# Performance work log

Measured on AMD Instinct MI355X. Metric: run time of the kernel, lower is better.

Reference implementation:

```python
import jax, jax.numpy as jnp
import numpy as np

N = 100000   # num_nodes
E = 300000   # num_edges
R = 200      # num_rels
B = 32       # num_bases (bdd blocks)
H = 128      # h_dim
SI = H // B  # submat_in = 4


def setup_inputs() -> dict:
    key = jax.random.key(0)
    ks = jax.random.split(key, 10)
    return {
        "node_ids": jnp.arange(N, dtype=jnp.int32),
        "src": jax.random.randint(ks[0], (E,), 0, N, dtype=jnp.int32),
        "dst": jax.random.randint(ks[1], (E,), 0, N, dtype=jnp.int32),
        "etypes": jax.random.randint(ks[2], (E,), 0, R, dtype=jnp.int32),
        "norm": jax.random.uniform(ks[3], (E, 1), dtype=jnp.float32),
        "emb": jax.random.normal(ks[4], (N, H), dtype=jnp.float32) * 0.02,
        "W1": jax.random.normal(ks[5], (R, B, SI, SI), dtype=jnp.float32) / np.float32(np.sqrt(SI)),
        "loop_w1": jax.random.normal(ks[6], (H, H), dtype=jnp.float32) / np.float32(np.sqrt(H)),
        "bias1": jnp.zeros((H,), dtype=jnp.float32),
        "W2": jax.random.normal(ks[7], (R, B, SI, 2 * SI), dtype=jnp.float32) / np.float32(np.sqrt(SI)),
        "loop_w2": jax.random.normal(ks[8], (H, 2 * H), dtype=jnp.float32) / np.float32(np.sqrt(H)),
        "bias2": jnp.zeros((2 * H,), dtype=jnp.float32),
        "eps": jax.random.normal(ks[9], (N, H), dtype=jnp.float32),
    }


def rel_graph_conv_bdd(h, src, dst, etypes, norm, W, loop_w, bias):
    """DGL RelGraphConv with regularizer='bdd', self_loop=True, bias=True."""
    _, Bb, si, so = W.shape
    h_src = h[src].reshape(-1, Bb, si)                  # (E, B, si)
    We = W[etypes]                                      # (E, B, si, so) gathered block weights
    msg = jnp.einsum('ebi,ebio->ebo', h_src, We).reshape(-1, Bb * so)  # (E, out)
    msg = msg * norm                                    # edge norm
    agg = jax.ops.segment_sum(msg, dst, num_segments=N)  # scatter-add to dst
    return agg + bias + h @ loop_w


def reference(node_ids, src, dst, etypes, norm, emb, W1, loop_w1, bias1, W2, loop_w2, bias2, eps):
    h = emb[node_ids]                                   # embedding lookup (N, H)
    h = jax.nn.relu(rel_graph_conv_bdd(h, src, dst, etypes, norm, W1, loop_w1, bias1))
    h = rel_graph_conv_bdd(h, src, dst, etypes, norm, W2, loop_w2, bias2)  # (N, 2H)
    # utils.gaussian_parameters: split last dim, v = softplus + 1e-8
    m, h_pre = jnp.split(h, 2, axis=-1)
    v = jax.nn.softplus(h_pre) + 1e-8
    # utils.sample_gaussian: reparameterized sample
    z = m + jnp.sqrt(v) * eps
    return z
```

## Files before the change

### kernel.cpp

```cpp
#include <hip/hip_runtime.h>
#include <math.h>

#define HD 128

union F4 { float4 v; float f[4]; };

typedef __attribute__((ext_vector_type(8))) short bf8_t;
typedef __attribute__((ext_vector_type(4))) float f4_t;

__device__ __forceinline__ unsigned short f2bf(float f){
  unsigned int u = __float_as_uint(f);
  return (unsigned short)((u + 0x7fffu + ((u>>16)&1u)) >> 16);
}

__device__ __forceinline__ float dotbf(const F4& h, unsigned int ua, unsigned int ub){
  float w0 = __uint_as_float(ua << 16);
  float w1 = __uint_as_float(ua & 0xffff0000u);
  float w2 = __uint_as_float(ub << 16);
  float w3 = __uint_as_float(ub & 0xffff0000u);
  return fmaf(h.f[0], w0, fmaf(h.f[1], w1, fmaf(h.f[2], w2, h.f[3]*w3)));
}

__device__ __forceinline__ void wpack_one(const float* __restrict__ W,
                                          unsigned short* __restrict__ Wp, int t, int NO){
  int lane = t & 63, ks = (t>>6) & 3, ct = t >> 8;
  int k0 = ks*32 + (lane>>4)*8, col = ct*16 + (lane&15);
  unsigned short v[8];
  #pragma unroll
  for (int j=0;j<8;++j) v[j] = f2bf(W[(k0+j)*NO + col]);
  ushort4* dst = (ushort4*)&Wp[(size_t)t*8];
  dst[0] = make_ushort4(v[0],v[1],v[2],v[3]);
  dst[1] = make_ushort4(v[4],v[5],v[6],v[7]);
}

__global__ void k_prep(const int* __restrict__ ids, const float4* __restrict__ emb4,
                       float4* __restrict__ h0, unsigned short* __restrict__ h0b,
                       const int* __restrict__ dst, int* __restrict__ counts,
                       const float* __restrict__ W1, unsigned short* __restrict__ W1Tb,
                       const float* __restrict__ W2, unsigned short* __restrict__ W2Tb,
                       const float* __restrict__ lw1, unsigned short* __restrict__ W1p,
                       const float* __restrict__ lw2, unsigned short* __restrict__ W2p,
                       int NG, int E, int n1, int n2){
  int i = blockIdx.x*256 + threadIdx.x;
  if (i < NG){
    int row = i>>5, c = i&31;
    float4 v = emb4[ids[row]*32 + c];
    h0[i] = v;
    *(ushort4*)&h0b[(size_t)i*4] = make_ushort4(f2bf(v.x),f2bf(v.y),f2bf(v.z),f2bf(v.w));
    return;
  }
  i -= NG;
  if (i < E){ atomicAdd(&counts[dst[i]], 1); return; }
  i -= E;
  if (i < n1){
    int ii = i & 3, o = (i>>2) & 3, rb = i>>4;
    W1Tb[i] = f2bf(W1[rb*16 + ii*4 + o]);
    return;
  }
  i -= n1;
  if (i < n2){
    int ii = i & 3, o = (i>>2) & 7, rb = i>>5;
    W2Tb[i] = f2bf(W2[rb*32 + ii*8 + o]);
    return;
  }
  i -= n2;
  if (i < 2048){ wpack_one(lw1, W1p, i, 128); return; }
  i -= 2048;
  if (i < 4096){ wpack_one(lw2, W2p, i, 256); }
}

__global__ void k_scan_block(const int* __restrict__ counts, int* __restrict__ scanTmp,
                             int* __restrict__ blockSums, int n){
  __shared__ int sm[256];
  int i = blockIdx.x*256 + threadIdx.x;
  int v = (i<n)?counts[i]:0;
  sm[threadIdx.x]=v; __syncthreads();
  for (int ofs=1; ofs<256; ofs<<=1){
    int t = (threadIdx.x>=ofs)?sm[threadIdx.x-ofs]:0;
    __syncthreads();
    sm[threadIdx.x]+=t;
    __syncthreads();
  }
  if (i<n) scanTmp[i]=sm[threadIdx.x];
  if (threadIdx.x==255) blockSums[blockIdx.x]=sm[255];
}

__global__ void k_scan_top(int* __restrict__ blockSums, int nb){
  __shared__ int sm[1024];
  int v = ((int)threadIdx.x<nb)?blockSums[threadIdx.x]:0;
  sm[threadIdx.x]=v; __syncthreads();
  for (int ofs=1; ofs<1024; ofs<<=1){
    int t = ((int)threadIdx.x>=ofs)?sm[threadIdx.x-ofs]:0;
    __syncthreads();
    sm[threadIdx.x]+=t;
    __syncthreads();
  }
  if ((int)threadIdx.x<nb) blockSums[threadIdx.x] = sm[threadIdx.x]-v;
}

__global__ void k_scan_fin(const int* __restrict__ scanTmp, const int* __restrict__ blockSums,
                           const int* __restrict__ counts,
                           int* __restrict__ row_ptr, int* __restrict__ cursors, int n){
  int i = blockIdx.x*256 + threadIdx.x;
  if (i<n){
    int incl = scanTmp[i] + blockSums[blockIdx.x];
    row_ptr[i+1] = incl;
    cursors[i] = incl - counts[i];
  }
  if (i==0) row_ptr[0]=0;
}

__global__ void k_scatter(const int* __restrict__ dst, const int* __restrict__ src,
                          const int* __restrict__ et, const float* __restrict__ norm,
                          int* __restrict__ cursors, int4* __restrict__ pay, int E){
  int e = blockIdx.x*256 + threadIdx.x;
  if (e<E){
    int p = atomicAdd(&cursors[dst[e]],1);
    pay[p] = make_int4(src[e], et[e], __float_as_int(norm[e]), 0);
  }
}

__global__ __launch_bounds__(256)
void k_edge1(const int* __restrict__ row_ptr, const int4* __restrict__ pay,
             const float* __restrict__ h, const unsigned short* __restrict__ WTb,
             float* __restrict__ agg, int Nn){
  int wid = __builtin_amdgcn_readfirstlane((blockIdx.x*256 + threadIdx.x)>>6);
  if (wid >= Nn) return;
  const int lane = threadIdx.x & 63;
  const int half = lane >> 5, b = lane & 31;
  const int e0 = row_ptr[wid], e1 = row_ptr[wid+1];
  float a0=0.f, a1=0.f, a2=0.f, a3=0.f;
  int e = e0 + half;
  int4 p;
  if (e < e1) p = pay[e];
  for (; e < e1; e += 2){
    int4 pn = (e+2 < e1) ? pay[e+2] : p;
    float nm = __int_as_float(p.z);
    F4 hv; hv.v = *(const float4*)&h[(size_t)p.x*HD + b*4];
    const uint4* wq = (const uint4*)&WTb[(size_t)p.y*512 + b*16];
    uint4 q0 = wq[0], q1 = wq[1];
    a0 = fmaf(nm, dotbf(hv, q0.x, q0.y), a0);
    a1 = fmaf(nm, dotbf(hv, q0.z, q0.w), a1);
    a2 = fmaf(nm, dotbf(hv, q1.x, q1.y), a2);
    a3 = fmaf(nm, dotbf(hv, q1.z, q1.w), a3);
    p = pn;
  }
  a0 += __shfl_xor(a0, 32); a1 += __shfl_xor(a1, 32);
  a2 += __shfl_xor(a2, 32); a3 += __shfl_xor(a3, 32);
  if (half == 0){
    F4 o; o.f[0]=a0; o.f[1]=a1; o.f[2]=a2; o.f[3]=a3;
    *(float4*)&agg[(size_t)wid*128 + b*4] = o.v;
  }
}

__global__ __launch_bounds__(256)
void k_edge2(const int* __restrict__ row_ptr, const int4* __restrict__ pay,
             const float* __restrict__ h, const unsigned short* __restrict__ WTb,
             float* __restrict__ agg, int Nn){
  int wid = __builtin_amdgcn_readfirstlane((blockIdx.x*256 + threadIdx.x)>>6);
  if (wid >= Nn) return;
  const int lane = threadIdx.x & 63;
  const int half = lane >> 5, b = lane & 31;
  const int e0 = row_ptr[wid], e1 = row_ptr[wid+1];
  float acc[8];
  #pragma unroll
  for (int o=0;o<8;++o) acc[o]=0.f;
  int e = e0 + half;
  int4 p;
  if (e < e1) p = pay[e];
  for (; e < e1; e += 2){
    int4 pn = (e+2 < e1) ? pay[e+2] : p;
    float nm = __int_as_float(p.z);
    F4 hv; hv.v = *(const float4*)&h[(size_t)p.x*HD + b*4];
    const uint4* wq = (const uint4*)&WTb[(size_t)p.y*1024 + b*32];
    uint4 q0 = wq[0], q1 = wq[1], q2 = wq[2], q3 = wq[3];
    acc[0] = fmaf(nm, dotbf(hv, q0.x, q0.y), acc[0]);
    acc[1] = fmaf(nm, dotbf(hv, q0.z, q0.w), acc[1]);
    acc[2] = fmaf(nm, dotbf(hv, q1.x, q1.y), acc[2]);
    acc[3] = fmaf(nm, dotbf(hv, q1.z, q1.w), acc[3]);
    acc[4] = fmaf(nm, dotbf(hv, q2.x, q2.y), acc[4]);
    acc[5] = fmaf(nm, dotbf(hv, q2.z, q2.w), acc[5]);
    acc[6] = fmaf(nm, dotbf(hv, q3.x, q3.y), acc[6]);
    acc[7] = fmaf(nm, dotbf(hv, q3.z, q3.w), acc[7]);
    p = pn;
  }
  #pragma unroll
  for (int o=0;o<8;++o) acc[o] += __shfl_xor(acc[o], 32);
  if (half == 0){
    F4 o0, o1;
    #pragma unroll
    for (int j=0;j<4;++j){ o0.f[j]=acc[j]; o1.f[j]=acc[4+j]; }
    *(float4*)&agg[(size_t)wid*256 + b*8]     = o0.v;
    *(float4*)&agg[(size_t)wid*256 + b*8 + 4] = o1.v;
  }
}

__global__ __launch_bounds__(256)
void k_mfma_relu(const unsigned short* __restrict__ Ab, const unsigned short* __restrict__ Wp,
                 const float* __restrict__ agg, const float* __restrict__ bias,
                 float* __restrict__ out, unsigned short* __restrict__ outb, int M){
  const int lane = threadIdx.x & 63;
  const int rowBase = blockIdx.x*64 + (threadIdx.x>>6)*16;
  const int ar = lane & 15, kg = lane >> 4;
  const int aclamp = min(rowBase + ar, M-1);
  f4_t acc[8];
  #pragma unroll
  for (int ct=0; ct<8; ++ct) acc[ct] = (f4_t)0.f;
  #pragma unroll
  for (int ks=0; ks<4; ++ks){
    bf8_t a = *(const bf8_t*)&Ab[(size_t)aclamp*HD + ks*32 + kg*8];
    #pragma unroll
    for (int ct=0; ct<8; ++ct){
      bf8_t b = *(const bf8_t*)&Wp[(size_t)((ct*4 + ks)*64 + lane)*8];
      acc[ct] = __builtin_amdgcn_mfma_f32_16x16x32_bf16(a, b, acc[ct], 0,0,0);
    }
  }
  const int crow = rowBase + kg*4;
  #pragma unroll
  for (int r=0; r<4; ++r){
    int gr = crow + r;
    if (gr >= M) continue;
    #pragma unroll
    for (int ct=0; ct<8; ++ct){
      int col = ct*16 + ar;
      float v = fmaxf(acc[ct][r] + agg[(size_t)gr*128 + col] + bias[col], 0.f);
      out[(size_t)gr*128 + col] = v;
      outb[(size_t)gr*128 + col] = f2bf(v);
    }
  }
}

__global__ __launch_bounds__(256)
void k_mfma_gauss(const unsigned short* __restrict__ Ab, const unsigned short* __restrict__ Wp,
                  const float* __restrict__ agg, const float* __restrict__ bias,
                  const float* __restrict__ eps, float* __restrict__ out, int M){
  const int lane = threadIdx.x & 63;
  const int bx = blockIdx.x & 1;
  const int rowBase = (blockIdx.x>>1)*64 + (threadIdx.x>>6)*16;
  const int ar = lane & 15, kg = lane >> 4;
  const int aclamp = min(rowBase + ar, M-1);
  f4_t accm[4], acch[4];
  #pragma unroll
  for (int ct=0; ct<4; ++ct){ accm[ct] = (f4_t)0.f; acch[ct] = (f4_t)0.f; }
  #pragma unroll
  for (int ks=0; ks<4; ++ks){
    bf8_t a = *(const bf8_t*)&Ab[(size_t)aclamp*HD + ks*32 + kg*8];
    #pragma unroll
    for (int ct=0; ct<4; ++ct){
      int ctm = bx*4 + ct, cth = 8 + bx*4 + ct;
      bf8_t bm = *(const bf8_t*)&Wp[(size_t)((ctm*4 + ks)*64 + lane)*8];
      bf8_t bh = *(const bf8_t*)&Wp[(size_t)((cth*4 + ks)*64 + lane)*8];
      accm[ct] = __builtin_amdgcn_mfma_f32_16x16x32_bf16(a, bm, accm[ct], 0,0,0);
      acch[ct] = __builtin_amdgcn_mfma_f32_16x16x32_bf16(a, bh, acch[ct], 0,0,0);
    }
  }
  const int crow = rowBase + kg*4;
  #pragma unroll
  for (int r=0; r<4; ++r){
    int gr = crow + r;
    if (gr >= M) continue;
    #pragma unroll
    for (int ct=0; ct<4; ++ct){
      int colm = bx*64 + ct*16 + ar;
      float m  = accm[ct][r] + agg[(size_t)gr*256 + colm]       + bias[colm];
      float hp = acch[ct][r] + agg[(size_t)gr*256 + colm + 128] + bias[colm+128];
      float sp = fmaxf(hp, 0.f) + log1pf(expf(-fabsf(hp)));
      out[(size_t)gr*128 + colm] = fmaf(sqrtf(sp + 1e-8f), eps[(size_t)gr*128 + colm], m);
    }
  }
}

extern "C" void kernel_launch(void* const* d_in, const int* in_sizes, int n_in,
                              void* d_out, int out_size, void* d_ws, size_t ws_size,
                              hipStream_t stream){
  (void)n_in; (void)out_size; (void)ws_size;
  const int*   node_ids = (const int*)d_in[0];
  const int*   src  = (const int*)d_in[1];
  const int*   dst  = (const int*)d_in[2];
  const int*   et   = (const int*)d_in[3];
  const float* norm = (const float*)d_in[4];
  const float* emb  = (const float*)d_in[5];
  const float* W1   = (const float*)d_in[6];
  const float* lw1  = (const float*)d_in[7];
  const float* b1   = (const float*)d_in[8];
  const float* W2   = (const float*)d_in[9];
  const float* lw2  = (const float*)d_in[10];
  const float* b2   = (const float*)d_in[11];
  const float* eps  = (const float*)d_in[12];
  float* out = (float*)d_out;

  const int N  = in_sizes[0];
  const int E  = in_sizes[1];
  const int n1 = in_sizes[6];
  const int n2 = in_sizes[9];

  char* w = (char*)d_ws;
  size_t szNH = (size_t)N*HD*sizeof(float);
  float* h0   = (float*)(w);
  float* agg2 = (float*)(w);
  float* h1   = (float*)(w + 2*szNH);
  float* agg1 = (float*)(w + 3*szNH);
  char*  ip   = w + 4*szNH;
  int4*  pay       = (int4*)ip;
  int*   counts    = (int*)(pay + E);
  int*   scanTmp   = counts + N;
  int*   row_ptr   = scanTmp + N;
  int*   cursors   = row_ptr + (N+1);
  int*   blockSums = cursors + N;
  size_t tail      = ((size_t)((char*)(blockSums + 1024) - w) + 63) & ~(size_t)63;
  unsigned short* W1Tb = (unsigned short*)(w + tail);
  unsigned short* W2Tb = W1Tb + n1;
  unsigned short* W1p  = W2Tb + n2;
  unsigned short* W2p  = W1p + 8*256*8;
  unsigned short* h0b  = W2p + 16*256*8;
  unsigned short* h1b  = h0b + (size_t)N*HD;

  hipMemsetAsync(counts, 0, (size_t)N*sizeof(int), stream);

  const int NG = N*32;
  const int Tprep = NG + E + n1 + n2 + 2048 + 4096;
  int nb_e    = (E+255)/256;
  int nb_scan = (N+255)/256;

  k_prep<<<(Tprep+255)/256, 256, 0, stream>>>(node_ids, (const float4*)emb, (float4*)h0, h0b,
                                              dst, counts, W1, W1Tb, W2, W2Tb,
                                              lw1, W1p, lw2, W2p, NG, E, n1, n2);
  k_scan_block<<<nb_scan, 256, 0, stream>>>(counts, scanTmp, blockSums, N);
  k_scan_top<<<1, 1024, 0, stream>>>(blockSums, nb_scan);
  k_scan_fin<<<nb_scan, 256, 0, stream>>>(scanTmp, blockSums, counts, row_ptr, cursors, N);
  k_scatter<<<nb_e, 256, 0, stream>>>(dst, src, et, norm, cursors, pay, E);

  int nb_rows = (N+3)/4;
  int nb_m    = (N+63)/64;

  k_edge1<<<nb_rows, 256, 0, stream>>>(row_ptr, pay, h0, W1Tb, agg1, N);
  k_mfma_relu<<<nb_m, 256, 0, stream>>>(h0b, W1p, agg1, b1, h1, h1b, N);
  k_edge2<<<nb_rows, 256, 0, stream>>>(row_ptr, pay, h1, W2Tb, agg2, N);
  k_mfma_gauss<<<nb_m*2, 256, 0, stream>>>(h1b, W2p, agg2, b2, eps, out, N);
}
```

Baseline: 435.4 us.

## Gather bf16 node features in edge kernels and process four edges per wave

The edge kernels now gather the bf16 copy of the node features instead of the fp32 copy. The fp32 h0/h1 buffers are no longer written, which removes a full fp32 write per layer and halves the bytes read per gathered row. The per-wave mapping changes from 2 edges × 32 lanes (4 channels each) to 4 edges × 16 lanes (8 channels each), with a two-step shuffle reduction. This trades some feature precision (bf16 instead of fp32 input to the messages) and adds more registers and weight loads per lane.

New measurement: 434.4 us. Within noise of the previous version (-0.2%).

```diff
diff --git a/kernel.cpp b/kernel.cpp
--- a/kernel.cpp
+++ b/kernel.cpp
@@ -12,13 +12,11 @@
   unsigned int u = __float_as_uint(f);
   return (unsigned short)((u + 0x7fffu + ((u>>16)&1u)) >> 16);
 }
+__device__ __forceinline__ float bflo(unsigned int u){ return __uint_as_float(u << 16); }
+__device__ __forceinline__ float bfhi(unsigned int u){ return __uint_as_float(u & 0xffff0000u); }
 
 __device__ __forceinline__ float dotbf(const F4& h, unsigned int ua, unsigned int ub){
-  float w0 = __uint_as_float(ua << 16);
-  float w1 = __uint_as_float(ua & 0xffff0000u);
-  float w2 = __uint_as_float(ub << 16);
-  float w3 = __uint_as_float(ub & 0xffff0000u);
-  return fmaf(h.f[0], w0, fmaf(h.f[1], w1, fmaf(h.f[2], w2, h.f[3]*w3)));
+  return fmaf(h.f[0], bflo(ua), fmaf(h.f[1], bfhi(ua), fmaf(h.f[2], bflo(ub), h.f[3]*bfhi(ub))));
 }
 
 __device__ __forceinline__ void wpack_one(const float* __restrict__ W,
@@ -34,7 +32,7 @@
 }
 
 __global__ void k_prep(const int* __restrict__ ids, const float4* __restrict__ emb4,
-                       float4* __restrict__ h0, unsigned short* __restrict__ h0b,
+                       unsigned short* __restrict__ h0b,
                        const int* __restrict__ dst, int* __restrict__ counts,
                        const float* __restrict__ W1, unsigned short* __restrict__ W1Tb,
                        const float* __restrict__ W2, unsigned short* __restrict__ W2Tb,
@@ -45,7 +43,6 @@
   if (i < NG){
     int row = i>>5, c = i&31;
     float4 v = emb4[ids[row]*32 + c];
-    h0[i] = v;
     *(ushort4*)&h0b[(size_t)i*4] = make_ushort4(f2bf(v.x),f2bf(v.y),f2bf(v.z),f2bf(v.w));
     return;
   }
@@ -122,83 +119,115 @@
 
 __global__ __launch_bounds__(256)
 void k_edge1(const int* __restrict__ row_ptr, const int4* __restrict__ pay,
-             const float* __restrict__ h, const unsigned short* __restrict__ WTb,
+             const unsigned short* __restrict__ h, const unsigned short* __restrict__ WTb,
              float* __restrict__ agg, int Nn){
   int wid = __builtin_amdgcn_readfirstlane((blockIdx.x*256 + threadIdx.x)>>6);
   if (wid >= Nn) return;
   const int lane = threadIdx.x & 63;
-  const int half = lane >> 5, b = lane & 31;
+  const int g = lane >> 4, l = lane & 15;
   const int e0 = row_ptr[wid], e1 = row_ptr[wid+1];
-  float a0=0.f, a1=0.f, a2=0.f, a3=0.f;
-  int e = e0 + half;
+  const int cnt = e1 - e0;
+  float acc[8];
+  #pragma unroll
+  for (int o=0;o<8;++o) acc[o]=0.f;
+  const int T = (cnt + 3) >> 2;
   int4 p;
-  if (e < e1) p = pay[e];
-  for (; e < e1; e += 2){
-    int4 pn = (e+2 < e1) ? pay[e+2] : p;
-    float nm = __int_as_float(p.z);
-    F4 hv; hv.v = *(const float4*)&h[(size_t)p.x*HD + b*4];
-    const uint4* wq = (const uint4*)&WTb[(size_t)p.y*512 + b*16];
-    uint4 q0 = wq[0], q1 = wq[1];
-    a0 = fmaf(nm, dotbf(hv, q0.x, q0.y), a0);
-    a1 = fmaf(nm, dotbf(hv, q0.z, q0.w), a1);
-    a2 = fmaf(nm, dotbf(hv, q1.x, q1.y), a2);
-    a3 = fmaf(nm, dotbf(hv, q1.z, q1.w), a3);
+  if (cnt > 0) p = pay[min(e0 + g, e1-1)];
+  for (int it=0; it<T; ++it){
+    int base = e0 + it*4 + g;
+    float nm = (base < e1) ? __int_as_float(p.z) : 0.f;
+    int4 pn = p;
+    if (it+1 < T) pn = pay[min(base + 4, e1-1)];
+    uint4 hq = *(const uint4*)&h[(size_t)p.x*HD + l*8];
+    const uint4* wq = (const uint4*)&WTb[(size_t)p.y*512 + l*32];
+    uint4 w0 = wq[0], w1 = wq[1], w2 = wq[2], w3 = wq[3];
+    F4 hlo, hhi;
+    hlo.f[0]=bflo(hq.x); hlo.f[1]=bfhi(hq.x); hlo.f[2]=bflo(hq.y); hlo.f[3]=bfhi(hq.y);
+    hhi.f[0]=bflo(hq.z); hhi.f[1]=bfhi(hq.z); hhi.f[2]=bflo(hq.w); hhi.f[3]=bfhi(hq.w);
+    acc[0]=fmaf(nm, dotbf(hlo,w0.x,w0.y), acc[0]);
+    acc[1]=fmaf(nm, dotbf(hlo,w0.z,w0.w), acc[1]);
+    acc[2]=fmaf(nm, dotbf(hlo,w1.x,w1.y), acc[2]);
+    acc[3]=fmaf(nm, dotbf(hlo,w1.z,w1.w), acc[3]);
+    acc[4]=fmaf(nm, dotbf(hhi,w2.x,w2.y), acc[4]);
+    acc[5]=fmaf(nm, dotbf(hhi,w2.z,w2.w), acc[5]);
+    acc[6]=fmaf(nm, dotbf(hhi,w3.x,w3.y), acc[6]);
+    acc[7]=fmaf(nm, dotbf(hhi,w3.z,w3.w), acc[7]);
     p = pn;
   }
-  a0 += __shfl_xor(a0, 32); a1 += __shfl_xor(a1, 32);
-  a2 += __shfl_xor(a2, 32); a3 += __shfl_xor(a3, 32);
-  if (half == 0){
-    F4 o; o.f[0]=a0; o.f[1]=a1; o.f[2]=a2; o.f[3]=a3;
-    *(float4*)&agg[(size_t)wid*128 + b*4] = o.v;
+  #pragma unroll
+  for (int o=0;o<8;++o){ acc[o] += __shfl_xor(acc[o],16); acc[o] += __shfl_xor(acc[o],32); }
+  if (g == 0){
+    F4 o0, o1;
+    #pragma unroll
+    for (int j=0;j<4;++j){ o0.f[j]=acc[j]; o1.f[j]=acc[4+j]; }
+    *(float4*)&agg[(size_t)wid*128 + l*8]     = o0.v;
+    *(float4*)&agg[(size_t)wid*128 + l*8 + 4] = o1.v;
   }
 }
 
 __global__ __launch_bounds__(256)
 void k_edge2(const int* __restrict__ row_ptr, const int4* __restrict__ pay,
-             const float* __restrict__ h, const unsigned short* __restrict__ WTb,
+             const unsigned short* __restrict__ h, const unsigned short* __restrict__ WTb,
              float* __restrict__ agg, int Nn){
   int wid = __builtin_amdgcn_readfirstlane((blockIdx.x*256 + threadIdx.x)>>6);
   if (wid >= Nn) return;
   const int lane = threadIdx.x & 63;
-  const int half = lane >> 5, b = lane & 31;
+  const int g = lane >> 4, l = lane & 15;
   const int e0 = row_ptr[wid], e1 = row_ptr[wid+1];
-  float acc[8];
-  #pragma unroll
-  for (int o=0;o<8;++o) acc[o]=0.f;
-  int e = e0 + half;
+  const int cnt = e1 - e0;
+  float acc[16];
+  #pragma unroll
+  for (int o=0;o<16;++o) acc[o]=0.f;
+  const int T = (cnt + 3) >> 2;
   int4 p;
-  if (e < e1) p = pay[e];
-  for (; e < e1; e += 2){
-    int4 pn = (e+2 < e1) ? pay[e+2] : p;
-    float nm = __int_as_float(p.z);
-    F4 hv; hv.v = *(const float4*)&h[(size_t)p.x*HD + b*4];
-    const uint4* wq = (const uint4*)&WTb[(size_t)p.y*1024 + b*32];
-    uint4 q0 = wq[0], q1 = wq[1], q2 = wq[2], q3 = wq[3];
-    acc[0] = fmaf(nm, dotbf(hv, q0.x, q0.y), acc[0]);
-    acc[1] = fmaf(nm, dotbf(hv, q0.z, q0.w), acc[1]);
-    acc[2] = fmaf(nm, dotbf(hv, q1.x, q1.y), acc[2]);
-    acc[3] = fmaf(nm, dotbf(hv, q1.z, q1.w), acc[3]);
-    acc[4] = fmaf(nm, dotbf(hv, q2.x, q2.y), acc[4]);
-    acc[5] = fmaf(nm, dotbf(hv, q2.z, q2.w), acc[5]);
-    acc[6] = fmaf(nm, dotbf(hv, q3.x, q3.y), acc[6]);
-    acc[7] = fmaf(nm, dotbf(hv, q3.z, q3.w), acc[7]);
+  if (cnt > 0) p = pay[min(e0 + g, e1-1)];
+  for (int it=0; it<T; ++it){
+    int base = e0 + it*4 + g;
+    float nm = (base < e1) ? __int_as_float(p.z) : 0.f;
+    int4 pn = p;
+    if (it+1 < T) pn = pay[min(base + 4, e1-1)];
+    uint4 hq = *(const uint4*)&h[(size_t)p.x*HD + l*8];
+    const uint4* wq = (const uint4*)&WTb[(size_t)p.y*1024 + l*64];
+    uint4 wa0 = wq[0], wa1 = wq[1], wa2 = wq[2], wa3 = wq[3];
+    uint4 wb0 = wq[4], wb1 = wq[5], wb2 = wq[6], wb3 = wq[7];
+    F4 hlo, hhi;
+    hlo.f[0]=bflo(hq.x); hlo.f[1]=bfhi(hq.x); hlo.f[2]=bflo(hq.y); hlo.f[3]=bfhi(hq.y);
+    hhi.f[0]=bflo(hq.z); hhi.f[1]=bfhi(hq.z); hhi.f[2]=bflo(hq.w); hhi.f[3]=bfhi(hq.w);
+    acc[0] =fmaf(nm, dotbf(hlo,wa0.x,wa0.y), acc[0]);
+    acc[1] =fmaf(nm, dotbf(hlo,wa0.z,wa0.w), acc[1]);
+    acc[2] =fmaf(nm, dotbf(hlo,wa1.x,wa1.y), acc[2]);
+    acc[3] =fmaf(nm, dotbf(hlo,wa1.z,wa1.w), acc[3]);
+    acc[4] =fmaf(nm, dotbf(hlo,wa2.x,wa2.y), acc[4]);
+    acc[5] =fmaf(nm, dotbf(hlo,wa2.z,wa2.w), acc[5]);
+    acc[6] =fmaf(nm, dotbf(hlo,wa3.x,wa3.y), acc[6]);
+    acc[7] =fmaf(nm, dotbf(hlo,wa3.z,wa3.w), acc[7]);
+    acc[8] =fmaf(nm, dotbf(hhi,wb0.x,wb0.y), acc[8]);
+    acc[9] =fmaf(nm, dotbf(hhi,wb0.z,wb0.w), acc[9]);
+    acc[10]=fmaf(nm, dotbf(hhi,wb1.x,wb1.y), acc[10]);
+    acc[11]=fmaf(nm, dotbf(hhi,wb1.z,wb1.w), acc[11]);
+    acc[12]=fmaf(nm, dotbf(hhi,wb2.x,wb2.y), acc[12]);
+    acc[13]=fmaf(nm, dotbf(hhi,wb2.z,wb2.w), acc[13]);
+    acc[14]=fmaf(nm, dotbf(hhi,wb3.x,wb3.y), acc[14]);
+    acc[15]=fmaf(nm, dotbf(hhi,wb3.z,wb3.w), acc[15]);
     p = pn;
   }
   #pragma unroll
-  for (int o=0;o<8;++o) acc[o] += __shfl_xor(acc[o], 32);
-  if (half == 0){
-    F4 o0, o1;
-    #pragma unroll
-    for (int j=0;j<4;++j){ o0.f[j]=acc[j]; o1.f[j]=acc[4+j]; }
-    *(float4*)&agg[(size_t)wid*256 + b*8]     = o0.v;
-    *(float4*)&agg[(size_t)wid*256 + b*8 + 4] = o1.v;
+  for (int o=0;o<16;++o){ acc[o] += __shfl_xor(acc[o],16); acc[o] += __shfl_xor(acc[o],32); }
+  if (g == 0){
+    #pragma unroll
+    for (int q=0;q<4;++q){
+      F4 o;
+      #pragma unroll
+      for (int j=0;j<4;++j) o.f[j]=acc[q*4+j];
+      *(float4*)&agg[(size_t)wid*256 + l*16 + q*4] = o.v;
+    }
   }
 }
 
 __global__ __launch_bounds__(256)
 void k_mfma_relu(const unsigned short* __restrict__ Ab, const unsigned short* __restrict__ Wp,
                  const float* __restrict__ agg, const float* __restrict__ bias,
-                 float* __restrict__ out, unsigned short* __restrict__ outb, int M){
+                 unsigned short* __restrict__ outb, int M){
   const int lane = threadIdx.x & 63;
   const int rowBase = blockIdx.x*64 + (threadIdx.x>>6)*16;
   const int ar = lane & 15, kg = lane >> 4;
@@ -224,7 +253,6 @@
     for (int ct=0; ct<8; ++ct){
       int col = ct*16 + ar;
       float v = fmaxf(acc[ct][r] + agg[(size_t)gr*128 + col] + bias[col], 0.f);
-      out[(size_t)gr*128 + col] = v;
       outb[(size_t)gr*128 + col] = f2bf(v);
     }
   }
@@ -296,9 +324,7 @@
 
   char* w = (char*)d_ws;
   size_t szNH = (size_t)N*HD*sizeof(float);
-  float* h0   = (float*)(w);
   float* agg2 = (float*)(w);
-  float* h1   = (float*)(w + 2*szNH);
   float* agg1 = (float*)(w + 3*szNH);
   char*  ip   = w + 4*szNH;
   int4*  pay       = (int4*)ip;
@@ -322,7 +348,7 @@
   int nb_e    = (E+255)/256;
   int nb_scan = (N+255)/256;
 
-  k_prep<<<(Tprep+255)/256, 256, 0, stream>>>(node_ids, (const float4*)emb, (float4*)h0, h0b,
+  k_prep<<<(Tprep+255)/256, 256, 0, stream>>>(node_ids, (const float4*)emb, h0b,
                                               dst, counts, W1, W1Tb, W2, W2Tb,
                                               lw1, W1p, lw2, W2p, NG, E, n1, n2);
   k_scan_block<<<nb_scan, 256, 0, stream>>>(counts, scanTmp, blockSums, N);
@@ -333,8 +359,8 @@
   int nb_rows = (N+3)/4;
   int nb_m    = (N+63)/64;
 
-  k_edge1<<<nb_rows, 256, 0, stream>>>(row_ptr, pay, h0, W1Tb, agg1, N);
-  k_mfma_relu<<<nb_m, 256, 0, stream>>>(h0b, W1p, agg1, b1, h1, h1b, N);
-  k_edge2<<<nb_rows, 256, 0, stream>>>(row_ptr, pay, h1, W2Tb, agg2, N);
+  k_edge1<<<nb_rows, 256, 0, stream>>>(row_ptr, pay, h0b, W1Tb, agg1, N);
+  k_mfma_relu<<<nb_m, 256, 0, stream>>>(h0b, W1p, agg1, b1, h1b, N);
+  k_edge2<<<nb_rows, 256, 0, stream>>>(row_ptr, pay, h1b, W2Tb, agg2, N);
   k_mfma_gauss<<<nb_m*2, 256, 0, stream>>>(h1b, W2p, agg2, b2, eps, out, N);
 }
```
